# Optimization experiments

Hardware: AMD Instinct MI355X
Metric: run time of the kernel (lower is better)

The kernel has to match this reference:

```python
import jax, jax.numpy as jnp
import numpy as np

B, D, S, E = 256, 5, 30, 768
H1, H2, FF, OUT = 512, 512, 256, 2


def setup_inputs() -> dict:
    key = jax.random.key(0)
    ks = iter(jax.random.split(key, 40))

    def p(shape, scale=0.05):
        return jax.random.normal(next(ks), shape, jnp.float32) * scale

    return {
        "sentence_feats": jax.random.normal(next(ks), (B, D, S, E), jnp.float32),
        "time_feats": jax.random.uniform(next(ks), (B, D, S), jnp.float32),
        "len_tweets": jax.random.randint(next(ks), (B, D), 1, S + 1, jnp.int32),
        # TimeLSTM (lstm1)
        "Wd_w": p((H1, H1)), "Wd_b": p((H1,)),
        "Wall_w": p((4 * H1, H1)), "Wall_b": p((4 * H1,)),
        "Uall_w": p((4 * H1, E)), "Uall_b": p((4 * H1,)),
        # attn1
        "A1_W1_w": p((H1, H1)), "A1_W1_b": p((H1,)),
        "A1_W2_w": p((H1, H1)), "A1_W2_b": p((H1,)),
        "A1_V_w": p((1, H1)), "A1_V_b": p((1,)),
        # nn.LSTM (lstm2), gate order i,f,g,o
        "L2_Wih": p((4 * H2, H1)), "L2_Whh": p((4 * H2, H2)),
        "L2_bih": p((4 * H2,)), "L2_bhh": p((4 * H2,)),
        # attn2
        "A2_W1_w": p((H2, H2)), "A2_W1_b": p((H2,)),
        "A2_W2_w": p((H2, H2)), "A2_W2_b": p((H2,)),
        "A2_V_w": p((1, H2)), "A2_V_b": p((1,)),
        # head
        "lin3_w": p((FF, H2)), "lin3_b": p((FF,)),
        "lin4_w": p((OUT, FF)), "lin4_b": p((OUT,)),
    }


def _time_lstm(x, t, Wd_w, Wd_b, Wall_w, Wall_b, Uall_w, Uall_b):
    # x: (N,S,E), t: (N,S) -> o-gate outputs (N,S,H) (the torch module stacks `o`, not `h`)
    N = x.shape[0]
    H = Wd_w.shape[0]
    ux = jnp.einsum('nse,ge->nsg', x, Uall_w) + Uall_b  # (N,S,4H), hoisted out of recurrence

    def step(carry, inp):
        h, c = carry
        ux_s, t_s = inp
        c_s1 = jnp.tanh(c @ Wd_w.T + Wd_b)
        c_adj = c - c_s1 + c_s1 * t_s[:, None]
        gates = jax.nn.sigmoid(h @ Wall_w.T + Wall_b + ux_s)
        f, i, o, c_tmp = jnp.split(gates, 4, axis=1)  # all sigmoid, incl. c_tmp (as in source)
        c = f * c_adj + i * c_tmp
        h = o * jnp.tanh(c)
        return (h, c), o

    init = (jnp.zeros((N, H), x.dtype), jnp.zeros((N, H), x.dtype))
    _, os = jax.lax.scan(step, init, (ux.transpose(1, 0, 2), t.T))
    return os.transpose(1, 0, 2)  # (N,S,H)


def _std_lstm(x, Wih, Whh, bih, bhh):
    # PyTorch nn.LSTM, 1 layer, batch_first. x: (B,T,I) -> (hs (B,T,H), h_n (B,H))
    Bn = x.shape[0]
    H = Whh.shape[1]
    xi = jnp.einsum('bti,gi->btg', x, Wih) + bih + bhh  # (B,T,4H)

    def step(carry, xi_t):
        h, c = carry
        g = xi_t + h @ Whh.T
        i, f, gg, o = jnp.split(g, 4, axis=1)
        c = jax.nn.sigmoid(f) * c + jax.nn.sigmoid(i) * jnp.tanh(gg)
        h = jax.nn.sigmoid(o) * jnp.tanh(c)
        return (h, c), h

    init = (jnp.zeros((Bn, H), x.dtype), jnp.zeros((Bn, H), x.dtype))
    (h_n, _), hs = jax.lax.scan(step, init, xi.transpose(1, 0, 2))
    return hs.transpose(1, 0, 2), h_n


def _forward(sentence_feats, time_feats, Wd_w, Wd_b, Wall_w, Wall_b, Uall_w, Uall_b,
             A1_W1_w, A1_W1_b, A1_W2_w, A1_W2_b, A1_V_w, A1_V_b,
             L2_Wih, L2_Whh, L2_bih, L2_bhh,
             A2_W1_w, A2_W1_b, A2_W2_w, A2_W2_b, A2_V_w, A2_V_b,
             lin3_w, lin3_b, lin4_w, lin4_b, len_tweets):
    x = sentence_feats.transpose(1, 0, 2, 3)  # (D,B,S,E)
    t = time_feats.transpose(1, 0, 2)         # (D,B,S)
    lens = len_tweets.transpose(1, 0)          # (D,B)
    d, b, s, e = x.shape

    # run TimeLSTM over all days at once (days are independent, shared zero init)
    outs = _time_lstm(x.reshape(d * b, s, e), t.reshape(d * b, s),
                      Wd_w, Wd_b, Wall_w, Wall_b, Uall_w, Uall_b).reshape(d, b, s, H1)

    # Faithful to the source's inner loop: temp_hn ends up as the LAST batch
    # element's output at index len-1, shared across the whole batch of that day.
    idx = lens[:, -1] - 1  # (D,)
    last = jnp.take_along_axis(outs[:, -1], idx[:, None, None], axis=1)[:, 0]  # (D,H1)

    # attn1: score = V(tanh(W1(last) + W2(full))), mask by lens, softmax over S
    s1 = jnp.tanh((last @ A1_W1_w.T + A1_W1_b)[:, None, None, :]
                  + jnp.einsum('dbsh,gh->dbsg', outs, A1_W2_w) + A1_W2_b)
    score = jnp.einsum('dbsh,oh->dbso', s1, A1_V_w) + A1_V_b  # (D,B,S,1)
    mask = jnp.arange(s)[None, None, :] < lens[:, :, None]     # (D,B,S)
    score = jnp.where(mask[..., None], score, -jnp.inf)
    aw = jax.nn.softmax(score, axis=2)
    lstm1_out = jnp.sum(aw * outs, axis=2).transpose(1, 0, 2)  # (B,D,H1)

    lstm2_out, hn2 = _std_lstm(lstm1_out, L2_Wih, L2_Whh, L2_bih, L2_bhh)  # (B,D,H2),(B,H2)

    # attn2 over days
    s2 = jnp.tanh((hn2 @ A2_W1_w.T + A2_W1_b)[:, None, :]
                  + lstm2_out @ A2_W2_w.T + A2_W2_b)
    score2 = s2 @ A2_V_w.T + A2_V_b                 # (B,D,1)
    aw2 = jax.nn.softmax(score2, axis=1)
    ctx = jnp.sum(aw2 * lstm2_out, axis=1)          # (B,H2)

    h3 = jax.nn.relu(ctx @ lin3_w.T + lin3_b)       # dropout = identity (eval mode)
    return h3 @ lin4_w.T + lin4_b                   # (B,OUT)


def reference(sentence_feats, time_feats, len_tweets, Wd_w, Wd_b, Wall_w, Wall_b, Uall_w, Uall_b,
              A1_W1_w, A1_W1_b, A1_W2_w, A1_W2_b, A1_V_w, A1_V_b,
              L2_Wih, L2_Whh, L2_bih, L2_bhh,
              A2_W1_w, A2_W1_b, A2_W2_w, A2_W2_b, A2_V_w, A2_V_b,
              lin3_w, lin3_b, lin4_w, lin4_b):
    return _forward(sentence_feats, time_feats, Wd_w, Wd_b, Wall_w, Wall_b, Uall_w, Uall_b,
                    A1_W1_w, A1_W1_b, A1_W2_w, A1_W2_b, A1_V_w, A1_V_b,
                    L2_Wih, L2_Whh, L2_bih, L2_bhh,
                    A2_W1_w, A2_W1_b, A2_W2_w, A2_W2_b, A2_V_w, A2_V_b,
                    lin3_w, lin3_b, lin4_w, lin4_b, len_tweets)
```

## Files before the change

kernel.cpp:

```cpp
#include <hip/hip_runtime.h>
#include <math.h>

typedef _Float16 f16;
typedef _Float16 f16x4 __attribute__((ext_vector_type(4)));
typedef _Float16 f16x8 __attribute__((ext_vector_type(8)));
typedef float f32x4 __attribute__((ext_vector_type(4)));

#define DEV static __device__ __forceinline__

#define OFF_X16    ((size_t)0)
#define OFF_UX     ((size_t)58982400)
#define OFF_OUTS   ((size_t)216268800)
#define OFF_WD     ((size_t)255590400)
#define OFF_WALLP  ((size_t)256114688)
#define OFF_UP     ((size_t)258211840)
#define OFF_W2     ((size_t)261357568)
#define OFF_WIHP   ((size_t)261881856)
#define OFF_WHHP   ((size_t)263979008)
#define OFF_A2W1C  ((size_t)266076160)
#define OFF_A2W2C  ((size_t)266600448)
#define OFF_L3WC   ((size_t)267124736)
#define OFF_BALLP  ((size_t)267386880)
#define OFF_BIHP   ((size_t)267395072)
#define OFF_H16    ((size_t)267403264)
#define OFF_C16    ((size_t)270024704)
#define OFF_C32    ((size_t)272646144)
#define OFF_TFTN   ((size_t)277889024)
#define OFF_SCOREN (OFF_TFTN + 153600)
#define WS_NEED    (OFF_SCOREN + 153600)
#define OFF_W1L    ((size_t)153600)
#define OFF_L1O32  ((size_t)163840)
#define OFF_L1O16  ((size_t)2785280)
#define OFF_XI2    ((size_t)4096000)
#define OFF_C2     ((size_t)14581760)
#define OFF_H2     ((size_t)15630336)
#define OFF_L2O32  ((size_t)16154624)
#define OFF_L2O16  ((size_t)18776064)
#define OFF_U2     ((size_t)20086784)
#define OFF_V2     ((size_t)22708224)
#define OFF_CTX16  ((size_t)23232512)
#define OFF_H3     ((size_t)23494656)

DEV float sigf(float x) { return 1.f / (1.f + __expf(-x)); }
DEV float tanhfast(float x) { float e = __expf(2.f * x); return 1.f - 2.f / (e + 1.f); }
DEV int permrow(int c) { return (((c >> 4) & 3) << 9) | ((c >> 6) << 4) | (c & 15); }

DEV void gload16(const f16* g, f16x8* lds) {
  __builtin_amdgcn_global_load_lds((const __attribute__((address_space(1))) void*)g,
                                   (__attribute__((address_space(3))) void*)lds, 16, 0, 0);
}

DEV void gemm_core(const f16* __restrict__ A, const f16* __restrict__ Bt, int K,
                   int rowBase, int colBase, f16x8* sh, f32x4 (&acc)[4][4]) {
  const int t = threadIdx.x, lane = t & 63, w = t >> 6;
  const int wr = (w >> 1) * 64, wc = (w & 1) * 64;
  const f16* Arow = A + (size_t)rowBase * K;
  const f16* Brow = Bt + (size_t)colBase * K;
  auto stage = [&](f16x8* dstBase, const f16* src, int k0) {
#pragma unroll
    for (int i = 0; i < 4; ++i) {
      int c = i * 256 + t; int r = c >> 3; int cc = (c & 7) ^ (r & 7);
      gload16(src + (size_t)r * K + (k0 + cc * 8), dstBase + i * 256 + (t & 192));
    }
  };
  stage(sh, Arow, 0);
  stage(sh + 2048, Brow, 0);
  const int nk = K >> 6;
  for (int kt = 0; kt < nk; ++kt) {
    const int cur = kt & 1;
    if (kt + 1 < nk) {
      stage(sh + (cur ^ 1) * 1024, Arow, (kt + 1) * 64);
      stage(sh + 2048 + (cur ^ 1) * 1024, Brow, (kt + 1) * 64);
      asm volatile("s_waitcnt vmcnt(8)" ::: "memory");
    } else {
      asm volatile("s_waitcnt vmcnt(0)" ::: "memory");
    }
    __builtin_amdgcn_s_barrier();
    __builtin_amdgcn_sched_barrier(0);
    const f16x8* shA = sh + cur * 1024;
    const f16x8* shB = sh + 2048 + cur * 1024;
    const int rr = lane & 15, chb = lane >> 4;
#pragma unroll
    for (int kk = 0; kk < 2; ++kk) {
      const int ch = kk * 4 + chb;
      f16x8 af[4], bf[4];
#pragma unroll
      for (int m = 0; m < 4; ++m) { int row = wr + m * 16 + rr; af[m] = shA[row * 8 + (ch ^ (row & 7))]; }
#pragma unroll
      for (int n = 0; n < 4; ++n) { int row = wc + n * 16 + rr; bf[n] = shB[row * 8 + (ch ^ (row & 7))]; }
#pragma unroll
      for (int m = 0; m < 4; ++m)
#pragma unroll
        for (int n = 0; n < 4; ++n)
          acc[m][n] = __builtin_amdgcn_mfma_f32_16x16x32_f16(af[m], bf[n], acc[m][n], 0, 0, 0);
    }
    __builtin_amdgcn_sched_barrier(0);
    __builtin_amdgcn_s_barrier();
  }
}

DEV void gemm_core256(const f16* __restrict__ A, const f16* __restrict__ Bt, int K,
                      int rowBase, int colBase, f16x8 (&shA)[2][2048], f16x8 (&shB)[2][2048],
                      f32x4 (&acc)[8][4]) {
  const int t = threadIdx.x, lane = t & 63, w = t >> 6;
  const int wm = w >> 2, wn = w & 3;
  const f16* Arow = A + (size_t)rowBase * K;
  const f16* Brow = Bt + (size_t)colBase * K;
  auto stage = [&](f16x8* dst, const f16* src, int k0) {
#pragma unroll
    for (int i = 0; i < 4; ++i) {
      int c = i * 512 + t; int r = c >> 3; int cc = (c & 7) ^ (r & 7);
      gload16(src + (size_t)r * K + (k0 + cc * 8), dst + i * 512 + (t & 448));
    }
  };
  stage(shA[0], Arow, 0);
  stage(shB[0], Brow, 0);
  const int nk = K >> 6;
  for (int kt = 0; kt < nk; ++kt) {
    const int cur = kt & 1;
    if (kt + 1 < nk) {
      stage(shA[cur ^ 1], Arow, (kt + 1) * 64);
      stage(shB[cur ^ 1], Brow, (kt + 1) * 64);
      asm volatile("s_waitcnt vmcnt(8)" ::: "memory");
    } else {
      asm volatile("s_waitcnt vmcnt(0)" ::: "memory");
    }
    __builtin_amdgcn_s_barrier();
    __builtin_amdgcn_sched_barrier(0);
    const f16x8* pA = shA[cur];
    const f16x8* pB = shB[cur];
    const int rr = lane & 15, chb = lane >> 4;
#pragma unroll
    for (int kk = 0; kk < 2; ++kk) {
      const int ch = kk * 4 + chb;
      f16x8 bf[4];
#pragma unroll
      for (int n = 0; n < 4; ++n) { int row = wn * 64 + n * 16 + rr; bf[n] = pB[row * 8 + (ch ^ (row & 7))]; }
#pragma unroll
      for (int m = 0; m < 8; ++m) {
        int row = wm * 128 + m * 16 + rr;
        f16x8 af = pA[row * 8 + (ch ^ (row & 7))];
#pragma unroll
        for (int n = 0; n < 4; ++n)
          acc[m][n] = __builtin_amdgcn_mfma_f32_16x16x32_f16(af, bf[n], acc[m][n], 0, 0, 0);
      }
    }
    __builtin_amdgcn_sched_barrier(0);
    __builtin_amdgcn_s_barrier();
  }
}

__global__ __launch_bounds__(512, 1) void k_gemm256(const f16* __restrict__ A, const f16* __restrict__ Bt,
                                                    int K, int N, f16* __restrict__ C16) {
  __shared__ f16x8 shA[2][2048];
  __shared__ f16x8 shB[2][2048];
  const int rb = blockIdx.y * 256, cb = blockIdx.x * 256;
  f32x4 acc[8][4] = {};
  gemm_core256(A, Bt, K, rb, cb, shA, shB, acc);
  const int t = threadIdx.x, lane = t & 63, w = t >> 6;
  const int wm = w >> 2, wn = w & 3;
  const int ec = lane & 15, er = (lane >> 4) * 4;
#pragma unroll
  for (int m = 0; m < 8; ++m)
#pragma unroll
    for (int n = 0; n < 4; ++n) {
      const int c = cb + wn * 64 + n * 16 + ec;
#pragma unroll
      for (int j = 0; j < 4; ++j) {
        const int r = rb + wm * 128 + m * 16 + er + j;
        C16[(size_t)r * N + c] = (f16)acc[m][n][j];
      }
    }
}

__global__ __launch_bounds__(256, 2) void k_score(const f16* __restrict__ outs, const f16* __restrict__ W2t,
    const float* __restrict__ W2b, const float* __restrict__ w1l, const float* __restrict__ V,
    float* __restrict__ score) {
  __shared__ f16x8 sh[4096];
  const int rb = blockIdx.y * 128, cb = blockIdx.x * 128;
  f32x4 acc[4][4] = {};
  gemm_core(outs, W2t, 512, rb, cb, sh, acc);
  const int t = threadIdx.x, lane = t & 63, w = t >> 6;
  const int wr = (w >> 1) * 64, wc = (w & 1) * 64, ec = lane & 15, er = (lane >> 4) * 4;
  float* sacc = (float*)sh;
  if (t < 128) sacc[t] = 0.f;
  __syncthreads();
#pragma unroll
  for (int m = 0; m < 4; ++m)
#pragma unroll
    for (int j = 0; j < 4; ++j) {
      const int lr = wr + m * 16 + er + j;
      const int r = rb + lr;
      const int d = (r / 30) >> 8;
      float p = 0.f;
#pragma unroll
      for (int n = 0; n < 4; ++n) {
        const int c = cb + wc + n * 16 + ec;
        p += V[c] * tanhfast(acc[m][n][j] + W2b[c] + w1l[d * 512 + c]);
      }
      p += __shfl_xor(p, 1); p += __shfl_xor(p, 2); p += __shfl_xor(p, 4); p += __shfl_xor(p, 8);
      if (ec == 0) atomicAdd(&sacc[lr], p);
    }
  __syncthreads();
  if (t < 128) atomicAdd(&score[rb + t], sacc[t]);
}

template <int ACT, bool O32, bool O16>
__global__ __launch_bounds__(256, 2) void k_gemm(const f16* __restrict__ A, const f16* __restrict__ Bt,
                                                 int K, int N, const float* __restrict__ bias,
                                                 float* __restrict__ C32, f16* __restrict__ C16) {
  __shared__ f16x8 sh[4096];
  const int rb = blockIdx.y * 128, cb = blockIdx.x * 128;
  f32x4 acc[4][4] = {};
  gemm_core(A, Bt, K, rb, cb, sh, acc);
  const int t = threadIdx.x, lane = t & 63, w = t >> 6;
  const int wr = (w >> 1) * 64, wc = (w & 1) * 64, ec = lane & 15, er = (lane >> 4) * 4;
#pragma unroll
  for (int m = 0; m < 4; ++m)
#pragma unroll
    for (int n = 0; n < 4; ++n) {
      const int c = cb + wc + n * 16 + ec;
      const float bv = bias ? bias[c] : 0.f;
#pragma unroll
      for (int j = 0; j < 4; ++j) {
        const int r = rb + wr + m * 16 + er + j;
        float v = acc[m][n][j] + bv;
        if (ACT == 3) v = fmaxf(v, 0.f);
        if (O32) C32[(size_t)r * N + c] = v;
        if (O16) C16[(size_t)r * N + c] = (f16)v;
      }
    }
}

__global__ __launch_bounds__(256, 1) void k_stepm(
    const f16* __restrict__ hin, const f16* __restrict__ cin16, const float* __restrict__ cin32,
    const f16* __restrict__ Wallp, const f16* __restrict__ Wd16,
    const f16* __restrict__ ux, const float* __restrict__ ballp, const float* __restrict__ Wd_b,
    const float* __restrict__ tft,
    float* __restrict__ cout32, f16* __restrict__ cout16, f16* __restrict__ hout,
    f16* __restrict__ outs,
    const f16* __restrict__ x16s, const f16* __restrict__ U16p, f16* __restrict__ uxout, int s) {
  __shared__ f16x8 shAll[9728];
  const int bid = (int)blockIdx.x;
  const int t = threadIdx.x, lane = t & 63, w = t >> 6;
  const int wr = (w >> 1) * 64, wc = (w & 1) * 64;
  const int ec = lane & 15, er = (lane >> 4) * 4;

  if (bid >= 160) {
    const int q = bid - 160;
    const int slab = s + 2;
    const int rbu = (q >> 4) * 128, cbu = (q & 15) * 128;
    f32x4 acc[4][4] = {};
    gemm_core(x16s + (size_t)slab * 1280 * 768, U16p, 768, rbu, cbu, shAll, acc);
    f16* C = uxout + (size_t)slab * 1280 * 2048;
#pragma unroll
    for (int m = 0; m < 4; ++m)
#pragma unroll
      for (int n = 0; n < 4; ++n) {
        const int c = cbu + wc + n * 16 + ec;
#pragma unroll
        for (int j = 0; j < 4; ++j)
          C[(size_t)(rbu + wr + m * 16 + er + j) * 2048 + c] = (f16)acc[m][n][j];
      }
    return;
  }

  f16x8* shA = shAll;
  f16x8* shB = shAll + 2048;
  f16x8* shC = shAll + 4096;
  f16x8* shD = shAll + 6144;
  f16x8* shU = shAll + 6656;
  f16x8* shE = shAll + 8704;
  const int rb = (bid >> 4) * 128;
  const int cg = bid & 15;
  const int rr = lane & 15, chb = lane >> 4;
  const int h = cg * 32 + (w & 1) * 16 + ec;
  const int hcol = (w & 1) * 16 + ec;
  const f16* Ah = hin + (size_t)rb * 512;
  const f16* Ac = cin16 + (size_t)rb * 512;
  const f16* Bw = Wallp + (size_t)cg * 128 * 512;
  const f16* Bd = Wd16 + (size_t)cg * 32 * 512;
  const f16* uxs = ux + (size_t)s * 1280 * 2048;
  float bW[4];
#pragma unroll
  for (int n = 0; n < 4; ++n) bW[n] = ballp[cg * 128 + wc + n * 16 + ec];
  const float bD = Wd_b[h];
  const f16* shUf = (const f16*)shU;
  const float* shEf = (const float*)shE;
  const int kbase = (wc >> 3) + (ec >> 3);
  f32x4 acc[4][4] = {};
  f32x4 acc2[4] = {};

  auto stage128 = [&](f16x8* dstBase, const f16* src, int k0) {
#pragma unroll
    for (int i = 0; i < 4; ++i) {
      int c = i * 256 + t; int r = c >> 3; int cc = (c & 7) ^ (r & 7);
      gload16(src + (size_t)r * 512 + (k0 + cc * 8), dstBase + i * 256 + (t & 192));
    }
  };
  auto stage32 = [&](f16x8* dstBase, const f16* src, int k0) {
    const int r = t >> 3; const int cc = (t & 7) ^ (r & 7);
    gload16(src + (size_t)r * 512 + (k0 + cc * 8), dstBase + (t & 192));
  };
  auto stageU = [&]() {
#pragma unroll
    for (int i = 0; i < 8; ++i) {
      int c = i * 256 + t; int lr = c >> 4; int k = c & 15;
      int klog = k ^ (((lr >> 2) & 3) << 1);
      gload16(uxs + (size_t)(rb + lr) * 2048 + cg * 128 + klog * 8, shU + i * 256 + (t & 192));
    }
  };
  auto stageE = [&]() {
#pragma unroll
    for (int i = 0; i < 4; ++i) {
      int c = i * 256 + t; int lr = c >> 3; int k = c & 7;
      int klog = k ^ (((lr >> 2) & 1) << 2);
      gload16((const f16*)(cin32 + (size_t)(rb + lr) * 512 + cg * 32 + klog * 4),
              shE + i * 256 + (t & 192));
    }
  };

  if (s == 0) {
    stageU();
    stageE();
    asm volatile("s_waitcnt vmcnt(0)" ::: "memory");
    __builtin_amdgcn_s_barrier();
  } else {
    stage128(shA, Ah, 0);
    stage128(shB, Bw, 0);
    stage128(shC, Ac, 0);
    stage32(shD, Bd, 0);
    for (int kt = 0; kt < 8; ++kt) {
      const int cur = kt & 1;
      if (kt < 7) {
        stage128(shA + (cur ^ 1) * 1024, Ah, (kt + 1) * 64);
        stage128(shB + (cur ^ 1) * 1024, Bw, (kt + 1) * 64);
        stage128(shC + (cur ^ 1) * 1024, Ac, (kt + 1) * 64);
        stage32(shD + (cur ^ 1) * 256, Bd, (kt + 1) * 64);
        if (kt == 0) { stageU(); stageE(); }
        if (kt < 2) {
          asm volatile("s_waitcnt vmcnt(25)" ::: "memory");
        } else {
          asm volatile("s_waitcnt vmcnt(13)" ::: "memory");
        }
      } else {
        asm volatile("s_waitcnt vmcnt(0)" ::: "memory");
      }
      __builtin_amdgcn_s_barrier();
      __builtin_amdgcn_sched_barrier(0);
      const f16x8* pA = shA + cur * 1024;
      const f16x8* pB = shB + cur * 1024;
      const f16x8* pC = shC + cur * 1024;
      const f16x8* pD = shD + cur * 256;
#pragma unroll
      for (int kk = 0; kk < 2; ++kk) {
        const int ch = kk * 4 + chb;
        f16x8 af[4], bf[4], cf[4], df;
#pragma unroll
        for (int m = 0; m < 4; ++m) {
          const int row = wr + m * 16 + rr;
          af[m] = pA[row * 8 + (ch ^ (row & 7))];
          cf[m] = pC[row * 8 + (ch ^ (row & 7))];
        }
#pragma unroll
        for (int n = 0; n < 4; ++n) { const int row = wc + n * 16 + rr; bf[n] = pB[row * 8 + (ch ^ (row & 7))]; }
        { const int row = (w & 1) * 16 + rr; df = pD[row * 8 + (ch ^ (row & 7))]; }
#pragma unroll
        for (int m = 0; m < 4; ++m) {
#pragma unroll
          for (int n = 0; n < 4; ++n)
            acc[m][n] = __builtin_amdgcn_mfma_f32_16x16x32_f16(af[m], bf[n], acc[m][n], 0, 0, 0);
          acc2[m] = __builtin_amdgcn_mfma_f32_16x16x32_f16(cf[m], df, acc2[m], 0, 0, 0);
        }
      }
      __builtin_amdgcn_sched_barrier(0);
      __builtin_amdgcn_s_barrier();
    }
  }

#pragma unroll
  for (int m = 0; m < 4; ++m)
#pragma unroll
    for (int j = 0; j < 4; ++j) {
      const int lr = wr + m * 16 + er + j;
      const int r = rb + lr;
      const float tv = tft[s * 1280 + r];
      const int sU = ((lr >> 2) & 3) << 1;
      const float u0 = (float)shUf[(lr * 16 + ((kbase + 0) ^ sU)) * 8 + (ec & 7)];
      const float u1 = (float)shUf[(lr * 16 + ((kbase + 2) ^ sU)) * 8 + (ec & 7)];
      const float u2v = (float)shUf[(lr * 16 + ((kbase + 4) ^ sU)) * 8 + (ec & 7)];
      const float u3 = (float)shUf[(lr * 16 + ((kbase + 6) ^ sU)) * 8 + (ec & 7)];
      const float p0 = acc[m][0][j] + bW[0] + u0;
      const float p1 = acc[m][1][j] + bW[1] + u1;
      const float p2 = acc[m][2][j] + bW[2] + u2v;
      const float p3 = acc[m][3][j] + bW[3] + u3;
      const float f = sigf(p0), i = sigf(p1), o = sigf(p2), ct = sigf(p3);
      const float cs = tanhfast(acc2[m][j] + bD);
      const int sE = ((lr >> 2) & 1) << 2;
      const float c_old = shEf[(lr * 8 + ((hcol >> 2) ^ sE)) * 4 + (hcol & 3)];
      const float cadj = c_old - cs + cs * tv;
      const float cn = f * cadj + i * ct;
      cout32[(size_t)r * 512 + h] = cn;
      cout16[(size_t)r * 512 + h] = (f16)cn;
      hout[(size_t)r * 512 + h] = (f16)(o * tanhfast(cn));
      outs[((size_t)r * 30 + s) * 512 + h] = (f16)o;
    }
}

__global__ __launch_bounds__(256, 2) void k_l2step(const f16* __restrict__ hin, const f16* __restrict__ Whhp,
    const float* __restrict__ xi2, const float* __restrict__ cin, float* __restrict__ cout,
    f16* __restrict__ hout, float* __restrict__ l2o32, f16* __restrict__ l2o16, int ts) {
  __shared__ f16x8 sh[4096];
  const int rb = (blockIdx.x >> 4) * 128, cg = blockIdx.x & 15;
  f32x4 acc[4][4] = {};
  gemm_core(hin, Whhp, 512, rb, cg * 128, sh, acc);
  const int t = threadIdx.x, lane = t & 63, w = t >> 6;
  const int wr = (w >> 1) * 64, wc = (w & 1) * 64, ec = lane & 15, er = (lane >> 4) * 4;
  const int h = cg * 32 + (w & 1) * 16 + ec;
#pragma unroll
  for (int m = 0; m < 4; ++m)
#pragma unroll
    for (int j = 0; j < 4; ++j) {
      const int r = rb + wr + m * 16 + er + j;
      const size_t xb = ((size_t)r * 5 + ts) * 2048 + cg * 128 + wc + ec;
      const float p0 = acc[m][0][j] + xi2[xb];
      const float p1 = acc[m][1][j] + xi2[xb + 16];
      const float p2 = acc[m][2][j] + xi2[xb + 32];
      const float p3 = acc[m][3][j] + xi2[xb + 48];
      const float ii = sigf(p0), ff = sigf(p1), gg = tanhfast(p2), oo = sigf(p3);
      const float cn = ff * cin[(size_t)r * 512 + h] + ii * gg;
      const float hn = oo * tanhfast(cn);
      cout[(size_t)r * 512 + h] = cn;
      hout[(size_t)r * 512 + h] = (f16)hn;
      const size_t ob = ((size_t)r * 5 + ts) * 512 + h;
      l2o32[ob] = hn;
      l2o16[ob] = (f16)hn;
    }
}

__global__ __launch_bounds__(256) void k_w1last(const f16* __restrict__ outs, const int* __restrict__ lens,
                                                const float* __restrict__ W1, const float* __restrict__ W1b,
                                                float* __restrict__ w1l) {
  __shared__ float lastv[512];
  const int d = blockIdx.x;
  const int idx = lens[255 * 5 + d] - 1;
  const size_t row = ((size_t)(d * 256 + 255) * 30 + idx) * 512;
  for (int h = threadIdx.x; h < 512; h += 256) lastv[h] = (float)outs[row + h];
  __syncthreads();
  for (int h = threadIdx.x; h < 512; h += 256) {
    const float* wr = W1 + (size_t)h * 512;
    float p = W1b[h];
    for (int k = 0; k < 512; ++k) p += lastv[k] * wr[k];
    w1l[d * 512 + h] = p;
  }
}

__global__ __launch_bounds__(256) void k_attn1(const float* __restrict__ score, const f16* __restrict__ outs,
                                               const int* __restrict__ lens,
                                               float* __restrict__ l1o32, f16* __restrict__ l1o16) {
  __shared__ float saw[32];
  const int n = blockIdx.x;
  const int d = n >> 8, b = n & 255;
  const int len = lens[b * 5 + d];
  const int t = threadIdx.x, lane = t & 63, w = t >> 6;
  if (w == 0) {
    const bool valid = lane < len;
    float sc = valid ? score[(size_t)n * 30 + lane] : -INFINITY;
    float mx = sc;
#pragma unroll
    for (int off = 32; off > 0; off >>= 1) mx = fmaxf(mx, __shfl_xor(mx, off));
    float e = valid ? __expf(sc - mx) : 0.f;
    float sm = e;
#pragma unroll
    for (int off = 32; off > 0; off >>= 1) sm += __shfl_xor(sm, off);
    if (lane < 30) saw[lane] = e / sm;
  }
  __syncthreads();
  for (int h = t; h < 512; h += 256) {
    float acc = 0.f;
    for (int s = 0; s < len; ++s) acc += saw[s] * (float)outs[((size_t)n * 30 + s) * 512 + h];
    const size_t o = ((size_t)b * 5 + d) * 512 + h;
    l1o32[o] = acc;
    l1o16[o] = (f16)acc;
  }
}

__global__ __launch_bounds__(256, 2) void k_uv(const f16* __restrict__ l2o16, const f16* __restrict__ A2W2c,
    const f16* __restrict__ h2fin, const f16* __restrict__ A2W1c,
    const float* __restrict__ bu, const float* __restrict__ bv,
    float* __restrict__ u2, float* __restrict__ v2) {
  __shared__ f16x8 sh[4096];
  const int bid = blockIdx.x;
  const f16* A; const f16* B; const float* bias; float* out; int rb, cb;
  if (bid < 40) { A = l2o16; B = A2W2c; bias = bu; out = u2; rb = (bid >> 2) * 128; cb = (bid & 3) * 128; }
  else { int b2 = bid - 40; A = h2fin; B = A2W1c; bias = bv; out = v2; rb = (b2 >> 2) * 128; cb = (b2 & 3) * 128; }
  f32x4 acc[4][4] = {};
  gemm_core(A, B, 512, rb, cb, sh, acc);
  const int t = threadIdx.x, lane = t & 63, w = t >> 6;
  const int wr = (w >> 1) * 64, wc = (w & 1) * 64, ec = lane & 15, er = (lane >> 4) * 4;
#pragma unroll
  for (int m = 0; m < 4; ++m)
#pragma unroll
    for (int n = 0; n < 4; ++n) {
      const int c = cb + wc + n * 16 + ec;
      const float bvv = bias[c];
#pragma unroll
      for (int j = 0; j < 4; ++j) out[(size_t)(rb + wr + m * 16 + er + j) * 512 + c] = acc[m][n][j] + bvv;
    }
}

__global__ __launch_bounds__(256) void k_attn2(const float* __restrict__ u2, const float* __restrict__ v2,
                                               const float* __restrict__ l2o, const float* __restrict__ V2,
                                               const float* __restrict__ V2b, f16* __restrict__ ctx16) {
  __shared__ float ssc[8];
  __shared__ float saw[8];
  const int b = blockIdx.x;
  const int t = threadIdx.x, lane = t & 63, w = t >> 6;
  for (int tt = w; tt < 5; tt += 4) {
    const float* ur = u2 + ((size_t)b * 5 + tt) * 512;
    const float* vr = v2 + (size_t)b * 512;
    float p = 0.f;
#pragma unroll
    for (int j = 0; j < 8; ++j) { int h = lane * 8 + j; p += V2[h] * tanhfast(ur[h] + vr[h]); }
#pragma unroll
    for (int off = 32; off > 0; off >>= 1) p += __shfl_down(p, off);
    if (lane == 0) ssc[tt] = p + V2b[0];
  }
  __syncthreads();
  if (w == 0) {
    const bool valid = lane < 5;
    float sc = valid ? ssc[lane] : -INFINITY;
    float mx = sc;
#pragma unroll
    for (int off = 32; off > 0; off >>= 1) mx = fmaxf(mx, __shfl_xor(mx, off));
    float e = valid ? __expf(sc - mx) : 0.f;
    float sm = e;
#pragma unroll
    for (int off = 32; off > 0; off >>= 1) sm += __shfl_xor(sm, off);
    if (valid) saw[lane] = e / sm;
  }
  __syncthreads();
  for (int h = t; h < 512; h += 256) {
    float a = 0.f;
#pragma unroll
    for (int tt = 0; tt < 5; ++tt) a += saw[tt] * l2o[((size_t)b * 5 + tt) * 512 + h];
    ctx16[(size_t)b * 512 + h] = (f16)a;
  }
}

__global__ __launch_bounds__(256) void k_final(const float* __restrict__ h3, const float* __restrict__ W4,
                                               const float* __restrict__ b4, float* __restrict__ out) {
  const int idx = blockIdx.x * 256 + threadIdx.x;
  const int b = idx >> 1, o = idx & 1;
  const float* hr = h3 + b * 256;
  const float* wr = W4 + o * 256;
  float p = b4[o];
  for (int j = 0; j < 256; ++j) p += hr[j] * wr[j];
  out[idx] = p;
}

__global__ __launch_bounds__(256) void k_castx(const float* __restrict__ sf, f16* __restrict__ x16s) {
  const int total = 7372800;
  for (int e = blockIdx.x * 256 + threadIdx.x; e < total; e += gridDim.x * 256) {
    const int row = e / 192, k = e - row * 192;
    const int b = row / 150, rem = row - b * 150;
    const int d = rem / 30, s = rem - d * 30;
    const int orow = s * 1280 + d * 256 + b;
    const float4 v = ((const float4*)sf)[e];
    f16x4 o = {(f16)v.x, (f16)v.y, (f16)v.z, (f16)v.w};
    ((f16x4*)x16s)[(size_t)orow * 192 + k] = o;
  }
}

struct WPArgs { const float* src[9]; f16* dst[9]; int k4[9]; int cnt4[9]; int perm[9]; };
__global__ __launch_bounds__(256) void k_castwp(WPArgs a) {
  int g = blockIdx.x * 256 + threadIdx.x;
#pragma unroll
  for (int si = 0; si < 9; ++si) {
    if (g < a.cnt4[si]) {
      const int K4 = a.k4[si];
      const int c = g / K4, k = g - c * K4;
      const int srow = a.perm[si] ? permrow(c) : c;
      const float4 v = ((const float4*)a.src[si])[(size_t)srow * K4 + k];
      f16x4 o = {(f16)v.x, (f16)v.y, (f16)v.z, (f16)v.w};
      ((f16x4*)a.dst[si])[(size_t)c * K4 + k] = o;
      return;
    }
    g -= a.cnt4[si];
  }
}

__global__ __launch_bounds__(256) void k_zero(f16* h16a, f16* c16a, float* c32a,
    float* ballp, float* bihp, const float* Wall_b, const float* Uall_b,
    const float* bih, const float* bhh, float* tft, const float* tf,
    float* score, const float* Vb) {
  const int i = blockIdx.x * 256 + threadIdx.x;
  if (i < 655360) { h16a[i] = (f16)0.f; c16a[i] = (f16)0.f; c32a[i] = 0.f; }
  if (i < 2048) {
    const int p = permrow(i);
    ballp[i] = Wall_b[p] + Uall_b[p];
    bihp[i] = bih[p] + bhh[p];
  }
  if (i < 38400) {
    const int s = i / 1280, r = i - s * 1280;
    const int d = r >> 8, b = r & 255;
    tft[i] = tf[((size_t)b * 5 + d) * 30 + s];
    score[i] = Vb[0];
  }
}

__global__ __launch_bounds__(256) void k_init2(f16* h2a, float* c2a) {
  const int i = blockIdx.x * 256 + threadIdx.x;
  if (i < 131072) { h2a[i] = (f16)0.f; c2a[i] = 0.f; }
}

extern "C" void kernel_launch(void* const* d_in, const int* in_sizes, int n_in,
                              void* d_out, int out_size, void* d_ws, size_t ws_size,
                              hipStream_t stream) {
  const float* sf     = (const float*)d_in[0];
  const float* tf     = (const float*)d_in[1];
  const int*   lens   = (const int*)d_in[2];
  const float* Wd_w   = (const float*)d_in[3];
  const float* Wd_b   = (const float*)d_in[4];
  const float* Wall_w = (const float*)d_in[5];
  const float* Wall_b = (const float*)d_in[6];
  const float* Uall_w = (const float*)d_in[7];
  const float* Uall_b = (const float*)d_in[8];
  const float* A1W1   = (const float*)d_in[9];
  const float* A1W1b  = (const float*)d_in[10];
  const float* A1W2   = (const float*)d_in[11];
  const float* A1W2b  = (const float*)d_in[12];
  const float* A1V    = (const float*)d_in[13];
  const float* A1Vb   = (const float*)d_in[14];
  const float* Wih    = (const float*)d_in[15];
  const float* Whh    = (const float*)d_in[16];
  const float* bih    = (const float*)d_in[17];
  const float* bhh    = (const float*)d_in[18];
  const float* A2W1   = (const float*)d_in[19];
  const float* A2W1b  = (const float*)d_in[20];
  const float* A2W2   = (const float*)d_in[21];
  const float* A2W2b  = (const float*)d_in[22];
  const float* A2V    = (const float*)d_in[23];
  const float* A2Vb   = (const float*)d_in[24];
  const float* L3w    = (const float*)d_in[25];
  const float* L3b    = (const float*)d_in[26];
  const float* L4w    = (const float*)d_in[27];
  const float* L4b    = (const float*)d_in[28];

  if (ws_size < WS_NEED) return;
  char* ws = (char*)d_ws;
  f16*   x16s   = (f16*)(ws + OFF_X16);
  f16*   ux16   = (f16*)(ws + OFF_UX);
  f16*   outs16 = (f16*)(ws + OFF_OUTS);
  f16*   Wd16   = (f16*)(ws + OFF_WD);
  f16*   Wallp  = (f16*)(ws + OFF_WALLP);
  f16*   U16p   = (f16*)(ws + OFF_UP);
  f16*   W216   = (f16*)(ws + OFF_W2);
  f16*   Wihp   = (f16*)(ws + OFF_WIHP);
  f16*   Whhp   = (f16*)(ws + OFF_WHHP);
  f16*   A2W116 = (f16*)(ws + OFF_A2W1C);
  f16*   A2W216 = (f16*)(ws + OFF_A2W2C);
  f16*   L316   = (f16*)(ws + OFF_L3WC);
  float* ballp  = (float*)(ws + OFF_BALLP);
  float* bihp   = (float*)(ws + OFF_BIHP);
  f16*   h16b[2]  = {(f16*)(ws + OFF_H16), (f16*)(ws + OFF_H16 + 1310720)};
  f16*   c16b[2]  = {(f16*)(ws + OFF_C16), (f16*)(ws + OFF_C16 + 1310720)};
  float* c32b[2]  = {(float*)(ws + OFF_C32), (float*)(ws + OFF_C32 + 2621440)};
  float* tft    = (float*)(ws + OFF_TFTN);
  float* score  = (float*)(ws + OFF_SCOREN);
  float* w1l    = (float*)(ws + OFF_W1L);
  float* l1o32  = (float*)(ws + OFF_L1O32);
  f16*   l1o16  = (f16*)(ws + OFF_L1O16);
  float* xi2    = (float*)(ws + OFF_XI2);
  float* c2b[2] = {(float*)(ws + OFF_C2), (float*)(ws + OFF_C2 + 524288)};
  f16*   h2b[2] = {(f16*)(ws + OFF_H2), (f16*)(ws + OFF_H2 + 262144)};
  float* l2o32  = (float*)(ws + OFF_L2O32);
  f16*   l2o16  = (f16*)(ws + OFF_L2O16);
  float* u2     = (float*)(ws + OFF_U2);
  float* v2     = (float*)(ws + OFF_V2);
  f16*   ctx16  = (f16*)(ws + OFF_CTX16);
  float* h3     = (float*)(ws + OFF_H3);

  k_castx<<<2048, 256, 0, stream>>>(sf, x16s);
  WPArgs wa;
  wa.src[0] = Wd_w;   wa.dst[0] = Wd16;   wa.k4[0] = 128; wa.cnt4[0] = 65536;  wa.perm[0] = 0;
  wa.src[1] = A1W2;   wa.dst[1] = W216;   wa.k4[1] = 128; wa.cnt4[1] = 65536;  wa.perm[1] = 0;
  wa.src[2] = A2W1;   wa.dst[2] = A2W116; wa.k4[2] = 128; wa.cnt4[2] = 65536;  wa.perm[2] = 0;
  wa.src[3] = A2W2;   wa.dst[3] = A2W216; wa.k4[3] = 128; wa.cnt4[3] = 65536;  wa.perm[3] = 0;
  wa.src[4] = L3w;    wa.dst[4] = L316;   wa.k4[4] = 128; wa.cnt4[4] = 32768;  wa.perm[4] = 0;
  wa.src[5] = Wall_w; wa.dst[5] = Wallp;  wa.k4[5] = 128; wa.cnt4[5] = 262144; wa.perm[5] = 1;
  wa.src[6] = Uall_w; wa.dst[6] = U16p;   wa.k4[6] = 192; wa.cnt4[6] = 393216; wa.perm[6] = 1;
  wa.src[7] = Wih;    wa.dst[7] = Wihp;   wa.k4[7] = 128; wa.cnt4[7] = 262144; wa.perm[7] = 1;
  wa.src[8] = Whh;    wa.dst[8] = Whhp;   wa.k4[8] = 128; wa.cnt4[8] = 262144; wa.perm[8] = 1;
  k_castwp<<<5760, 256, 0, stream>>>(wa);
  k_zero<<<2560, 256, 0, stream>>>(h16b[0], c16b[0], c32b[0], ballp, bihp, Wall_b, Uall_b, bih, bhh,
                                   tft, tf, score, A1Vb);

  k_gemm256<<<dim3(8, 10), 512, 0, stream>>>(x16s, U16p, 768, 2048, ux16);

  for (int s = 0; s < 30; ++s) {
    const int pi = s & 1, po = pi ^ 1;
    const int nb = (s <= 27) ? 320 : 160;
    k_stepm<<<nb, 256, 0, stream>>>(h16b[pi], c16b[pi], c32b[pi], Wallp, Wd16, ux16, ballp, Wd_b, tft,
                                    c32b[po], c16b[po], h16b[po], outs16,
                                    x16s, U16p, ux16, s);
  }

  k_init2<<<512, 256, 0, stream>>>(h2b[0], c2b[0]);

  k_w1last<<<5, 256, 0, stream>>>(outs16, lens, A1W1, A1W1b, w1l);
  k_score<<<dim3(4, 300), 256, 0, stream>>>(outs16, W216, A1W2b, w1l, A1V, score);
  k_attn1<<<1280, 256, 0, stream>>>(score, outs16, lens, l1o32, l1o16);

  k_gemm<0, true, false><<<dim3(16, 10), 256, 0, stream>>>(l1o16, Wihp, 512, 2048, bihp, xi2, nullptr);
  for (int ts = 0; ts < 5; ++ts) {
    const int pi = ts & 1, po = pi ^ 1;
    k_l2step<<<32, 256, 0, stream>>>(h2b[pi], Whhp, xi2, c2b[pi], c2b[po], h2b[po], l2o32, l2o16, ts);
  }

  k_uv<<<48, 256, 0, stream>>>(l2o16, A2W216, h2b[1], A2W116, A2W2b, A2W1b, u2, v2);
  k_attn2<<<256, 256, 0, stream>>>(u2, v2, l2o32, A2V, A2Vb, ctx16);

  k_gemm<3, true, false><<<dim3(2, 2), 256, 0, stream>>>(ctx16, L316, 512, 256, L3b, h3, nullptr);
  k_final<<<2, 256, 0, stream>>>(h3, L4w, L4b, (float*)d_out);
}
```

Measured before the change: 919.6 us.

## Widen side-GEMM tiles in step kernel to 128x256, halving extra blocks

The blocks inside the recurrent step kernel that precompute the next Ux slab now each produce a 128x256 output tile, using two B tiles that share one A tile, with an inline double-buffered pipeline. This halves the side-GEMM block count from 160 to 80, so each step launches 240 blocks instead of 320 and A-tile loads are reused across twice the columns. The cost is more accumulator registers and longer per-block work, which could stretch the step's critical path if those blocks finish after the recurrence blocks.

```diff
diff --git a/kernel.cpp b/kernel.cpp
--- a/kernel.cpp
+++ b/kernel.cpp
@@ -249,18 +249,77 @@
   if (bid >= 160) {
     const int q = bid - 160;
     const int slab = s + 2;
-    const int rbu = (q >> 4) * 128, cbu = (q & 15) * 128;
-    f32x4 acc[4][4] = {};
-    gemm_core(x16s + (size_t)slab * 1280 * 768, U16p, 768, rbu, cbu, shAll, acc);
+    const int rbu = (q >> 3) * 128;
+    const int cbu = (q & 7) * 256;
+    const f16* Au = x16s + (size_t)slab * 1280 * 768 + (size_t)rbu * 768;
+    const f16* B0 = U16p + (size_t)cbu * 768;
+    const f16* B1 = U16p + (size_t)(cbu + 128) * 768;
+    f16x8* sA  = shAll;
+    f16x8* sB0 = shAll + 2048;
+    f16x8* sB1 = shAll + 4096;
+    const int rr = lane & 15, chb = lane >> 4;
+    f32x4 acc0[4][4] = {};
+    f32x4 acc1[4][4] = {};
+    auto stageK = [&](f16x8* dst, const f16* src, int k0) {
+#pragma unroll
+      for (int i = 0; i < 4; ++i) {
+        int c = i * 256 + t; int r = c >> 3; int cc = (c & 7) ^ (r & 7);
+        gload16(src + (size_t)r * 768 + (k0 + cc * 8), dst + i * 256 + (t & 192));
+      }
+    };
+    stageK(sA, Au, 0);
+    stageK(sB0, B0, 0);
+    stageK(sB1, B1, 0);
+    for (int kt = 0; kt < 12; ++kt) {
+      const int cur = kt & 1;
+      if (kt < 11) {
+        stageK(sA + (cur ^ 1) * 1024, Au, (kt + 1) * 64);
+        stageK(sB0 + (cur ^ 1) * 1024, B0, (kt + 1) * 64);
+        stageK(sB1 + (cur ^ 1) * 1024, B1, (kt + 1) * 64);
+        asm volatile("s_waitcnt vmcnt(12)" ::: "memory");
+      } else {
+        asm volatile("s_waitcnt vmcnt(0)" ::: "memory");
+      }
+      __builtin_amdgcn_s_barrier();
+      __builtin_amdgcn_sched_barrier(0);
+      const f16x8* pA  = sA + cur * 1024;
+      const f16x8* pB0 = sB0 + cur * 1024;
+      const f16x8* pB1 = sB1 + cur * 1024;
+#pragma unroll
+      for (int kk = 0; kk < 2; ++kk) {
+        const int ch = kk * 4 + chb;
+        f16x8 af[4], bf0[4], bf1[4];
+#pragma unroll
+        for (int m = 0; m < 4; ++m) { int row = wr + m * 16 + rr; af[m] = pA[row * 8 + (ch ^ (row & 7))]; }
+#pragma unroll
+        for (int n = 0; n < 4; ++n) {
+          int row = wc + n * 16 + rr;
+          bf0[n] = pB0[row * 8 + (ch ^ (row & 7))];
+          bf1[n] = pB1[row * 8 + (ch ^ (row & 7))];
+        }
+#pragma unroll
+        for (int m = 0; m < 4; ++m)
+#pragma unroll
+          for (int n = 0; n < 4; ++n) {
+            acc0[m][n] = __builtin_amdgcn_mfma_f32_16x16x32_f16(af[m], bf0[n], acc0[m][n], 0, 0, 0);
+            acc1[m][n] = __builtin_amdgcn_mfma_f32_16x16x32_f16(af[m], bf1[n], acc1[m][n], 0, 0, 0);
+          }
+      }
+      __builtin_amdgcn_sched_barrier(0);
+      __builtin_amdgcn_s_barrier();
+    }
     f16* C = uxout + (size_t)slab * 1280 * 2048;
 #pragma unroll
     for (int m = 0; m < 4; ++m)
 #pragma unroll
       for (int n = 0; n < 4; ++n) {
-        const int c = cbu + wc + n * 16 + ec;
-#pragma unroll
-        for (int j = 0; j < 4; ++j)
-          C[(size_t)(rbu + wr + m * 16 + er + j) * 2048 + c] = (f16)acc[m][n][j];
+        const int c0 = cbu + wc + n * 16 + ec;
+#pragma unroll
+        for (int j = 0; j < 4; ++j) {
+          const size_t rowoff = (size_t)(rbu + wr + m * 16 + er + j) * 2048;
+          C[rowoff + c0] = (f16)acc0[m][n][j];
+          C[rowoff + c0 + 128] = (f16)acc1[m][n][j];
+        }
       }
     return;
   }
@@ -700,7 +759,7 @@
 
   for (int s = 0; s < 30; ++s) {
     const int pi = s & 1, po = pi ^ 1;
-    const int nb = (s <= 27) ? 320 : 160;
+    const int nb = (s <= 27) ? 240 : 160;
     k_stepm<<<nb, 256, 0, stream>>>(h16b[pi], c16b[pi], c32b[pi], Wallp, Wd16, ux16, ballp, Wd_b, tft,
                                     c32b[po], c16b[po], h16b[po], outs16,
                                     x16s, U16p, ux16, s);
```

Measured after the change: 950.9 us. 1.03x slower.
